# Optimization experiments

Hardware: AMD Instinct MI355X
Metric: run time of the kernel (lower is better)

The kernel has to match this reference:

```python
import jax, jax.numpy as jnp
import numpy as np

N = 100000
E = 1600000
D = 128   # path_code_size
H = 32    # GIN hidden dim (hard-coded in module)
BN_EPS = 1e-5
GIN_EPS = 0.0  # GINConv default eps


def gin_conv(x, src, dst, Wa, ba, Wb, bb, num_nodes):
    # sum-aggregate neighbor features: messages x[src] scattered to dst
    agg = jax.ops.segment_sum(x[src], dst, num_segments=num_nodes)
    h = (1.0 + GIN_EPS) * x + agg
    h = jax.nn.relu(h @ Wa + ba)
    return h @ Wb + bb


def batch_norm(x, gamma, beta):
    # training-mode BN over the node dimension (biased variance, like torch)
    mean = jnp.mean(x, axis=0)
    var = jnp.mean((x - mean) ** 2, axis=0)
    return (x - mean) * jax.lax.rsqrt(var + BN_EPS) * gamma + beta


def setup_inputs() -> dict:
    key = jax.random.key(0)
    ks = jax.random.split(key, 12)
    x = jax.random.normal(ks[0], (N, D), dtype=jnp.float32)
    edge_index = jax.random.randint(ks[1], (2, E), 0, N, dtype=jnp.int64)

    def lin(k, fan_in, fan_out):
        bound = 1.0 / np.sqrt(fan_in)
        kw, kb = jax.random.split(k)
        W = jax.random.uniform(kw, (fan_in, fan_out), jnp.float32, -bound, bound)
        b = jax.random.uniform(kb, (fan_out,), jnp.float32, -bound, bound)
        return W, b

    W1a, b1a = lin(ks[2], D, H)
    W1b, b1b = lin(ks[3], H, H)
    W2a, b2a = lin(ks[4], H, H)
    W2b, b2b = lin(ks[5], H, D)
    return {
        "x": x, "edge_index": edge_index,
        "W1a": W1a, "b1a": b1a, "W1b": W1b, "b1b": b1b,
        "g1": jnp.ones((H,), jnp.float32), "be1": jnp.zeros((H,), jnp.float32),
        "W2a": W2a, "b2a": b2a, "W2b": W2b, "b2b": b2b,
        "g2": jnp.ones((D,), jnp.float32), "be2": jnp.zeros((D,), jnp.float32),
    }


def reference(x, edge_index, W1a, b1a, W1b, b1b, g1, be1, W2a, b2a, W2b, b2b, g2, be2):
    src, dst = edge_index[0], edge_index[1]
    h = jax.nn.relu(gin_conv(x, src, dst, W1a, b1a, W1b, b1b, N))
    h = batch_norm(h, g1, be1)
    h = jax.nn.relu(gin_conv(h, src, dst, W2a, b2a, W2b, b2b, N))
    h = batch_norm(h, g2, be2)
    return h
```

## Files before the change

kernel.cpp:

```cpp
#include <hip/hip_runtime.h>

constexpr int NN  = 100000;
constexpr int NE  = 1600000;
constexpr int D   = 128;
constexpr int H   = 32;
constexpr int CAP = 64;

__global__ __launch_bounds__(256) void k_fill(const int* __restrict__ src,
                                              const int* __restrict__ dst,
                                              int* __restrict__ cnt,
                                              int* __restrict__ slots) {
    for (int e = blockIdx.x * blockDim.x + threadIdx.x; e < NE;
         e += gridDim.x * blockDim.x) {
        const int d = dst[e];
        const int pos = atomicAdd(&cnt[d], 1);
        if (pos < CAP) slots[d * CAP + pos] = src[e];
    }
}

__global__ __launch_bounds__(256) void k_xw1(const float* __restrict__ x,
                                             const float* __restrict__ W,
                                             float* __restrict__ z) {
    __shared__ float Wl[D * H];
    for (int i = threadIdx.x; i < D * H; i += blockDim.x) Wl[i] = W[i];
    __syncthreads();
    const int j = threadIdx.x & 31;
    const int g = threadIdx.x >> 5;
    const int groups = blockDim.x >> 5;
    for (int n = blockIdx.x * groups + g; n < NN; n += gridDim.x * groups) {
        const float4 xv = ((const float4*)(x + (size_t)n * D))[j];
        float acc = 0.f;
#pragma unroll
        for (int l = 0; l < 32; ++l) {
            acc = fmaf(__shfl(xv.x, l, 32), Wl[(4 * l + 0) * H + j], acc);
            acc = fmaf(__shfl(xv.y, l, 32), Wl[(4 * l + 1) * H + j], acc);
            acc = fmaf(__shfl(xv.z, l, 32), Wl[(4 * l + 2) * H + j], acc);
            acc = fmaf(__shfl(xv.w, l, 32), Wl[(4 * l + 3) * H + j], acc);
        }
        z[n * H + j] = acc;
    }
}

__global__ __launch_bounds__(256) void k_mlp1(const float* __restrict__ z,
                                              const int* __restrict__ cnt,
                                              const int* __restrict__ slots,
                                              const float* __restrict__ b1a,
                                              const float* __restrict__ W1b,
                                              const float* __restrict__ b1b,
                                              float* __restrict__ r1,
                                              float* __restrict__ gsum,
                                              float* __restrict__ gsq) {
    __shared__ float lsum[H], lsq[H];
    const int j = threadIdx.x & 31;
    float wc[H];
#pragma unroll
    for (int k = 0; k < H; ++k) wc[k] = W1b[k * H + j];
    if (threadIdx.x < H) { lsum[threadIdx.x] = 0.f; lsq[threadIdx.x] = 0.f; }
    __syncthreads();
    const int g = threadIdx.x >> 5;
    const int groups = blockDim.x >> 5;
    const float ba = b1a[j], bb = b1b[j];
    float psum = 0.f, psq = 0.f;
    for (int n = blockIdx.x * groups + g; n < NN; n += gridDim.x * groups) {
        float t = z[n * H + j] + ba;
        const int deg = min(cnt[n], CAP);
        const int* row = slots + n * CAP;
        int e = 0;
        for (; e + 4 <= deg; e += 4) {
            const int s0 = row[e], s1 = row[e + 1], s2 = row[e + 2], s3 = row[e + 3];
            const float a0 = z[s0 * H + j], a1 = z[s1 * H + j];
            const float a2 = z[s2 * H + j], a3 = z[s3 * H + j];
            t += (a0 + a1) + (a2 + a3);
        }
        for (; e < deg; ++e) t += z[row[e] * H + j];
        t = fmaxf(t, 0.f);
        float u = bb;
#pragma unroll
        for (int k = 0; k < H; ++k) u = fmaf(__shfl(t, k, 32), wc[k], u);
        const float r = fmaxf(u, 0.f);
        r1[n * H + j] = r;
        psum += r;
        psq = fmaf(r, r, psq);
    }
    atomicAdd(&lsum[j], psum);
    atomicAdd(&lsq[j], psq);
    __syncthreads();
    if (threadIdx.x < H) {
        atomicAdd(&gsum[threadIdx.x], lsum[threadIdx.x]);
        atomicAdd(&gsq[threadIdx.x], lsq[threadIdx.x]);
    }
}

__global__ void k_finalize(const float* __restrict__ gsum, const float* __restrict__ gsq,
                           const float* __restrict__ gamma, const float* __restrict__ beta,
                           float* __restrict__ scale, float* __restrict__ shift, int C) {
    const int j = threadIdx.x;
    if (j < C) {
        const float mean = gsum[j] * (1.f / NN);
        const float var  = gsq[j] * (1.f / NN) - mean * mean;
        const float sc   = gamma[j] * rsqrtf(var + 1e-5f);
        scale[j] = sc;
        shift[j] = beta[j] - mean * sc;
    }
}

__global__ __launch_bounds__(256) void k_bn_w2a(const float* __restrict__ r1,
                                                const float* __restrict__ scale,
                                                const float* __restrict__ shift,
                                                const float* __restrict__ W2a,
                                                float* __restrict__ z2) {
    const int j = threadIdx.x & 31;
    float wc[H];
#pragma unroll
    for (int k = 0; k < H; ++k) wc[k] = W2a[k * H + j];
    const int g = threadIdx.x >> 5;
    const int groups = blockDim.x >> 5;
    const float sc = scale[j], sh = shift[j];
    for (int n = blockIdx.x * groups + g; n < NN; n += gridDim.x * groups) {
        const float y = fmaf(r1[n * H + j], sc, sh);
        float u = 0.f;
#pragma unroll
        for (int k = 0; k < H; ++k) u = fmaf(__shfl(y, k, 32), wc[k], u);
        z2[n * H + j] = u;
    }
}

__global__ __launch_bounds__(256) void k_mlp2(const float* __restrict__ z2,
                                              const int* __restrict__ cnt,
                                              const int* __restrict__ slots,
                                              const float* __restrict__ b2a,
                                              const float* __restrict__ W2b,
                                              const float* __restrict__ b2b,
                                              float* __restrict__ out,
                                              float* __restrict__ gsum,
                                              float* __restrict__ gsq) {
    __shared__ float lsum[D], lsq[D];
    const int lane = threadIdx.x & 63;
    const int wid  = threadIdx.x >> 6;
    const int j32  = lane & 31;
    const int half = lane >> 5;
    float wc0[H], wc1[H];
#pragma unroll
    for (int k = 0; k < H; ++k) {
        wc0[k] = W2b[k * D + lane];
        wc1[k] = W2b[k * D + 64 + lane];
    }
    if (threadIdx.x < D) { lsum[threadIdx.x] = 0.f; lsq[threadIdx.x] = 0.f; }
    __syncthreads();
    const float ba  = b2a[j32];
    const float bb0 = b2b[lane], bb1 = b2b[64 + lane];
    float ps0 = 0.f, pq0 = 0.f, ps1 = 0.f, pq1 = 0.f;
    const int wavesTotal = (gridDim.x * blockDim.x) >> 6;
    for (int n = blockIdx.x * (blockDim.x >> 6) + wid; n < NN; n += wavesTotal) {
        float tp = (half == 0) ? (z2[n * H + j32] + ba) : 0.f;
        const int deg = min(cnt[n], CAP);
        const int* row = slots + n * CAP;
        for (int e = half; e < deg; e += 2) tp += z2[row[e] * H + j32];
        float t = tp + __shfl_xor(tp, 32);
        t = fmaxf(t, 0.f);
        float u0 = bb0, u1 = bb1;
#pragma unroll
        for (int k = 0; k < H; ++k) {
            const float tk = __shfl(t, k, 32);
            u0 = fmaf(tk, wc0[k], u0);
            u1 = fmaf(tk, wc1[k], u1);
        }
        const float r0 = fmaxf(u0, 0.f), r1v = fmaxf(u1, 0.f);
        out[(size_t)n * D + lane]      = r0;
        out[(size_t)n * D + 64 + lane] = r1v;
        ps0 += r0; pq0 = fmaf(r0, r0, pq0);
        ps1 += r1v; pq1 = fmaf(r1v, r1v, pq1);
    }
    atomicAdd(&lsum[lane], ps0);      atomicAdd(&lsq[lane], pq0);
    atomicAdd(&lsum[64 + lane], ps1); atomicAdd(&lsq[64 + lane], pq1);
    __syncthreads();
    if (threadIdx.x < D) {
        atomicAdd(&gsum[threadIdx.x], lsum[threadIdx.x]);
        atomicAdd(&gsq[threadIdx.x], lsq[threadIdx.x]);
    }
}

__global__ __launch_bounds__(256) void k_bn_out(float* __restrict__ out,
                                                const float* __restrict__ scale,
                                                const float* __restrict__ shift) {
    const int total = NN * D / 4;
    float4* o4 = (float4*)out;
    for (int i = blockIdx.x * blockDim.x + threadIdx.x; i < total;
         i += gridDim.x * blockDim.x) {
        float4 v = o4[i];
        const int c = (i & 31) * 4;
        v.x = fmaf(v.x, scale[c + 0], shift[c + 0]);
        v.y = fmaf(v.y, scale[c + 1], shift[c + 1]);
        v.z = fmaf(v.z, scale[c + 2], shift[c + 2]);
        v.w = fmaf(v.w, scale[c + 3], shift[c + 3]);
        o4[i] = v;
    }
}

extern "C" void kernel_launch(void* const* d_in, const int* in_sizes, int n_in,
                              void* d_out, int out_size, void* d_ws, size_t ws_size,
                              hipStream_t stream) {
    const float* x   = (const float*)d_in[0];
    const int*   ei  = (const int*)d_in[1];
    const float* W1a = (const float*)d_in[2];
    const float* b1a = (const float*)d_in[3];
    const float* W1b = (const float*)d_in[4];
    const float* b1b = (const float*)d_in[5];
    const float* g1  = (const float*)d_in[6];
    const float* be1 = (const float*)d_in[7];
    const float* W2a = (const float*)d_in[8];
    const float* b2a = (const float*)d_in[9];
    const float* W2b = (const float*)d_in[10];
    const float* b2b = (const float*)d_in[11];
    const float* g2  = (const float*)d_in[12];
    const float* be2 = (const float*)d_in[13];
    float* out = (float*)d_out;
    const int* src = ei;
    const int* dst = ei + NE;

    float* ws = (float*)d_ws;
    float* z   = ws;
    float* r1  = ws + (size_t)NN * H;
    int*   cnt = (int*)(ws + 2 * (size_t)NN * H);
    float* st  = ws + 2 * (size_t)NN * H + NN;
    int*   slots = (int*)(st + 640);
    float* gsum1 = st;        float* gsq1 = st + 32;
    float* sc1   = st + 64;   float* sh1  = st + 96;
    float* gsum2 = st + 128;  float* gsq2 = st + 256;
    float* sc2   = st + 384;  float* sh2  = st + 512;

    hipMemsetAsync(cnt, 0, (NN + 640) * sizeof(float), stream);

    k_fill<<<4096, 256, 0, stream>>>(src, dst, cnt, slots);

    k_xw1<<<2048, 256, 0, stream>>>(x, W1a, z);
    k_mlp1<<<2048, 256, 0, stream>>>(z, cnt, slots, b1a, W1b, b1b, r1, gsum1, gsq1);
    k_finalize<<<1, 128, 0, stream>>>(gsum1, gsq1, g1, be1, sc1, sh1, H);

    k_bn_w2a<<<2048, 256, 0, stream>>>(r1, sc1, sh1, W2a, z);
    k_mlp2<<<2048, 256, 0, stream>>>(z, cnt, slots, b2a, W2b, b2b, out, gsum2, gsq2);
    k_finalize<<<1, 128, 0, stream>>>(gsum2, gsq2, g2, be2, sc2, sh2, D);
    k_bn_out<<<2048, 256, 0, stream>>>(out, sc2, sh2);
}
```

Measured before the change: 596.1 us.

## Move weights to LDS, widen gather unrolls, and retune grid sizes

Weight matrices that were held in per-thread register arrays (W1b, W2a, W2b) are now staged in shared memory, which cuts register pressure and may allow higher occupancy. The x@W1a kernel drops its float4 load plus shuffle broadcast in favour of direct per-lane scalar reads of each x element. The neighbor gather loops read indices with int4 vector loads and unroll by 8 in mlp1 and by 4 strided in mlp2, so more loads are in flight. Grid sizes change for k_fill and k_mlp2. Scalar x reads and extra LDS traffic could cost more than they save.

```diff
diff --git a/kernel.cpp b/kernel.cpp
--- a/kernel.cpp
+++ b/kernel.cpp
@@ -5,6 +5,7 @@
 constexpr int D   = 128;
 constexpr int H   = 32;
 constexpr int CAP = 64;
+
 
 __global__ __launch_bounds__(256) void k_fill(const int* __restrict__ src,
                                               const int* __restrict__ dst,
@@ -28,15 +29,10 @@
     const int g = threadIdx.x >> 5;
     const int groups = blockDim.x >> 5;
     for (int n = blockIdx.x * groups + g; n < NN; n += gridDim.x * groups) {
-        const float4 xv = ((const float4*)(x + (size_t)n * D))[j];
+        const float* xr = x + (size_t)n * D;
         float acc = 0.f;
-#pragma unroll
-        for (int l = 0; l < 32; ++l) {
-            acc = fmaf(__shfl(xv.x, l, 32), Wl[(4 * l + 0) * H + j], acc);
-            acc = fmaf(__shfl(xv.y, l, 32), Wl[(4 * l + 1) * H + j], acc);
-            acc = fmaf(__shfl(xv.z, l, 32), Wl[(4 * l + 2) * H + j], acc);
-            acc = fmaf(__shfl(xv.w, l, 32), Wl[(4 * l + 3) * H + j], acc);
-        }
+#pragma unroll 8
+        for (int k = 0; k < D; ++k) acc = fmaf(xr[k], Wl[k * H + j], acc);
         z[n * H + j] = acc;
     }
 }
@@ -50,13 +46,12 @@
                                               float* __restrict__ r1,
                                               float* __restrict__ gsum,
                                               float* __restrict__ gsq) {
+    __shared__ float Wl[H * H];
     __shared__ float lsum[H], lsq[H];
+    for (int i = threadIdx.x; i < H * H; i += blockDim.x) Wl[i] = W1b[i];
+    if (threadIdx.x < H) { lsum[threadIdx.x] = 0.f; lsq[threadIdx.x] = 0.f; }
+    __syncthreads();
     const int j = threadIdx.x & 31;
-    float wc[H];
-#pragma unroll
-    for (int k = 0; k < H; ++k) wc[k] = W1b[k * H + j];
-    if (threadIdx.x < H) { lsum[threadIdx.x] = 0.f; lsq[threadIdx.x] = 0.f; }
-    __syncthreads();
     const int g = threadIdx.x >> 5;
     const int groups = blockDim.x >> 5;
     const float ba = b1a[j], bb = b1b[j];
@@ -66,17 +61,20 @@
         const int deg = min(cnt[n], CAP);
         const int* row = slots + n * CAP;
         int e = 0;
-        for (; e + 4 <= deg; e += 4) {
-            const int s0 = row[e], s1 = row[e + 1], s2 = row[e + 2], s3 = row[e + 3];
-            const float a0 = z[s0 * H + j], a1 = z[s1 * H + j];
-            const float a2 = z[s2 * H + j], a3 = z[s3 * H + j];
-            t += (a0 + a1) + (a2 + a3);
+        for (; e + 8 <= deg; e += 8) {
+            const int4 a = *(const int4*)(row + e);
+            const int4 b = *(const int4*)(row + e + 4);
+            const float t0 = z[a.x * H + j], t1 = z[a.y * H + j];
+            const float t2 = z[a.z * H + j], t3 = z[a.w * H + j];
+            const float t4 = z[b.x * H + j], t5 = z[b.y * H + j];
+            const float t6 = z[b.z * H + j], t7 = z[b.w * H + j];
+            t += ((t0 + t1) + (t2 + t3)) + ((t4 + t5) + (t6 + t7));
         }
         for (; e < deg; ++e) t += z[row[e] * H + j];
         t = fmaxf(t, 0.f);
         float u = bb;
 #pragma unroll
-        for (int k = 0; k < H; ++k) u = fmaf(__shfl(t, k, 32), wc[k], u);
+        for (int k = 0; k < H; ++k) u = fmaf(__shfl(t, k, 32), Wl[k * H + j], u);
         const float r = fmaxf(u, 0.f);
         r1[n * H + j] = r;
         psum += r;
@@ -109,10 +107,10 @@
                                                 const float* __restrict__ shift,
                                                 const float* __restrict__ W2a,
                                                 float* __restrict__ z2) {
+    __shared__ float Wl[H * H];
+    for (int i = threadIdx.x; i < H * H; i += blockDim.x) Wl[i] = W2a[i];
+    __syncthreads();
     const int j = threadIdx.x & 31;
-    float wc[H];
-#pragma unroll
-    for (int k = 0; k < H; ++k) wc[k] = W2a[k * H + j];
     const int g = threadIdx.x >> 5;
     const int groups = blockDim.x >> 5;
     const float sc = scale[j], sh = shift[j];
@@ -120,7 +118,7 @@
         const float y = fmaf(r1[n * H + j], sc, sh);
         float u = 0.f;
 #pragma unroll
-        for (int k = 0; k < H; ++k) u = fmaf(__shfl(y, k, 32), wc[k], u);
+        for (int k = 0; k < H; ++k) u = fmaf(__shfl(y, k, 32), Wl[k * H + j], u);
         z2[n * H + j] = u;
     }
 }
@@ -134,41 +132,45 @@
                                               float* __restrict__ out,
                                               float* __restrict__ gsum,
                                               float* __restrict__ gsq) {
+    __shared__ float Wl[H * D];
     __shared__ float lsum[D], lsq[D];
+    for (int i = threadIdx.x; i < H * D; i += blockDim.x) Wl[i] = W2b[i];
+    if (threadIdx.x < D) { lsum[threadIdx.x] = 0.f; lsq[threadIdx.x] = 0.f; }
+    __syncthreads();
     const int lane = threadIdx.x & 63;
     const int wid  = threadIdx.x >> 6;
-    const int j32  = lane & 31;
+    const int j    = lane & 31;
     const int half = lane >> 5;
-    float wc0[H], wc1[H];
-#pragma unroll
-    for (int k = 0; k < H; ++k) {
-        wc0[k] = W2b[k * D + lane];
-        wc1[k] = W2b[k * D + 64 + lane];
-    }
-    if (threadIdx.x < D) { lsum[threadIdx.x] = 0.f; lsq[threadIdx.x] = 0.f; }
-    __syncthreads();
-    const float ba  = b2a[j32];
+    const float ba  = b2a[j];
     const float bb0 = b2b[lane], bb1 = b2b[64 + lane];
     float ps0 = 0.f, pq0 = 0.f, ps1 = 0.f, pq1 = 0.f;
-    const int wavesTotal = (gridDim.x * blockDim.x) >> 6;
-    for (int n = blockIdx.x * (blockDim.x >> 6) + wid; n < NN; n += wavesTotal) {
-        float tp = (half == 0) ? (z2[n * H + j32] + ba) : 0.f;
+    const int nw = (gridDim.x * blockDim.x) >> 6;
+    for (int n = blockIdx.x * 4 + wid; n < NN; n += nw) {
+        const int* row = slots + n * CAP;
         const int deg = min(cnt[n], CAP);
-        const int* row = slots + n * CAP;
-        for (int e = half; e < deg; e += 2) tp += z2[row[e] * H + j32];
+        float tp = (half == 0) ? z2[n * H + j] + ba : 0.f;
+        int e = half;
+        for (; e + 6 < deg; e += 8) {
+            const int s0 = row[e],     s1 = row[e + 2];
+            const int s2 = row[e + 4], s3 = row[e + 6];
+            const float a0 = z2[s0 * H + j], a1 = z2[s1 * H + j];
+            const float a2 = z2[s2 * H + j], a3 = z2[s3 * H + j];
+            tp += (a0 + a1) + (a2 + a3);
+        }
+        for (; e < deg; e += 2) tp += z2[row[e] * H + j];
         float t = tp + __shfl_xor(tp, 32);
         t = fmaxf(t, 0.f);
         float u0 = bb0, u1 = bb1;
 #pragma unroll
         for (int k = 0; k < H; ++k) {
             const float tk = __shfl(t, k, 32);
-            u0 = fmaf(tk, wc0[k], u0);
-            u1 = fmaf(tk, wc1[k], u1);
+            u0 = fmaf(tk, Wl[k * D + lane], u0);
+            u1 = fmaf(tk, Wl[k * D + 64 + lane], u1);
         }
         const float r0 = fmaxf(u0, 0.f), r1v = fmaxf(u1, 0.f);
         out[(size_t)n * D + lane]      = r0;
         out[(size_t)n * D + 64 + lane] = r1v;
-        ps0 += r0; pq0 = fmaf(r0, r0, pq0);
+        ps0 += r0;  pq0 = fmaf(r0, r0, pq0);
         ps1 += r1v; pq1 = fmaf(r1v, r1v, pq1);
     }
     atomicAdd(&lsum[lane], ps0);      atomicAdd(&lsq[lane], pq0);
@@ -231,14 +233,14 @@
 
     hipMemsetAsync(cnt, 0, (NN + 640) * sizeof(float), stream);
 
-    k_fill<<<4096, 256, 0, stream>>>(src, dst, cnt, slots);
+    k_fill<<<2048, 256, 0, stream>>>(src, dst, cnt, slots);
 
     k_xw1<<<2048, 256, 0, stream>>>(x, W1a, z);
     k_mlp1<<<2048, 256, 0, stream>>>(z, cnt, slots, b1a, W1b, b1b, r1, gsum1, gsq1);
     k_finalize<<<1, 128, 0, stream>>>(gsum1, gsq1, g1, be1, sc1, sh1, H);
 
     k_bn_w2a<<<2048, 256, 0, stream>>>(r1, sc1, sh1, W2a, z);
-    k_mlp2<<<2048, 256, 0, stream>>>(z, cnt, slots, b2a, W2b, b2b, out, gsum2, gsq2);
+    k_mlp2<<<2500, 256, 0, stream>>>(z, cnt, slots, b2a, W2b, b2b, out, gsum2, gsq2);
     k_finalize<<<1, 128, 0, stream>>>(gsum2, gsq2, g2, be2, sc2, sh2, D);
     k_bn_out<<<2048, 256, 0, stream>>>(out, sc2, sh2);
 }
```

After: 587.6 us. Within noise of the previous version (-1.4%).
